# Performance work log

Hardware: AMD Instinct MI355X
Metric: run time of the kernel (lower is better)

Reference implementation:

```python
import jax, jax.numpy as jnp
import numpy as np


def setup_inputs() -> dict:
    key = jax.random.key(0)
    k1, k2 = jax.random.split(key)
    B, S, D = 8, 4096, 1024
    E, P = 8, 4
    x = jax.random.normal(k1, (B, S, D), dtype=jnp.float32)
    phi_kernel = jax.random.normal(k2, (D, E * P), dtype=jnp.float32) * (1.0 / np.sqrt(D))
    phi_bias = jnp.zeros((E * P,), dtype=jnp.float32)
    return {"x": x, "phi_kernel": phi_kernel, "phi_bias": phi_bias,
            "num_experts": E, "num_slots": P}


def reference(x, phi_kernel, phi_bias, num_experts, num_slots):
    B, S, D = x.shape
    E, P = num_experts, num_slots
    # phi logits: [B,S,E,P]
    phi_logits = (jnp.einsum('bsd,dk->bsk', x, phi_kernel) + phi_bias).reshape(B, S, E, P)
    # softmax over the sequence axis (each slot is a convex combo of tokens)
    phi_weights = jax.nn.softmax(phi_logits, axis=1)
    # soft slots: weighted sum over tokens -> [B,E,P,D] (fused, no [B,S,E,P,D] blowup)
    soft_slots = jnp.einsum('bsd,bsep->bepd', x, phi_weights)
    expert_inputs = soft_slots.reshape(B, E, P * D)
    expert_weights = jnp.full((B, S, E), 1.0 / E, dtype=x.dtype)
    expert_indices = jnp.broadcast_to(jnp.arange(E, dtype=jnp.int32)[None, None, :], (B, S, E))
    return (expert_weights, expert_indices, phi_weights, soft_slots, expert_inputs)
```

## Files before the change

kernel.cpp:

```cpp
#include <hip/hip_runtime.h>
#include <hip/hip_bf16.h>

#define B 8
#define S 4096
#define DD 1024
#define KK 32

template <int DSPLIT>
__global__ __launch_bounds__(256) void k1_logits(const float* __restrict__ x,
                                                 const float* __restrict__ phi,
                                                 float* __restrict__ lp) {
    constexpr int DCH = DD / DSPLIT;
    constexpr int NCH = DCH / 32;
    __shared__ float xt[128 * 36];

    const int bid = blockIdx.x;
    const int dq  = bid & (DSPLIT - 1);
    const int st  = (bid / DSPLIT) & 31;
    const int b   = bid / (DSPLIT * 32);
    const int s0  = st * 128;
    const int tid = threadIdx.x;
    const int kg  = __builtin_amdgcn_readfirstlane(tid >> 6);
    const int lane = tid & 63;

    float acc0[8], acc1[8];
#pragma unroll
    for (int j = 0; j < 8; ++j) { acc0[j] = 0.f; acc1[j] = 0.f; }

    const float* xb = x + ((size_t)(b * S + s0)) * DD + dq * DCH;

    for (int ch = 0; ch < NCH; ++ch) {
        __syncthreads();
#pragma unroll
        for (int i = 0; i < 4; ++i) {
            int f = tid + i * 256;
            int row = f >> 3;
            int c4 = f & 7;
            float4 v = *(const float4*)(xb + (size_t)row * DD + ch * 32 + c4 * 4);
            *(float4*)(xt + row * 36 + c4 * 4) = v;
        }
        __syncthreads();

        const float* pbase = phi + (size_t)(dq * DCH + ch * 32) * KK + kg * 8;
#pragma unroll
        for (int g = 0; g < 8; ++g) {
            float4 a0 = *(const float4*)(xt + lane * 36 + g * 4);
            float4 a1 = *(const float4*)(xt + (lane + 64) * 36 + g * 4);
            const float* a0p = &a0.x;
            const float* a1p = &a1.x;
#pragma unroll
            for (int dd = 0; dd < 4; ++dd) {
                const float* pr = pbase + (size_t)(g * 4 + dd) * KK;
                float4 pA = *(const float4*)(pr);
                float4 pB = *(const float4*)(pr + 4);
                float av0 = a0p[dd];
                float av1 = a1p[dd];
                acc0[0] += av0 * pA.x; acc0[1] += av0 * pA.y;
                acc0[2] += av0 * pA.z; acc0[3] += av0 * pA.w;
                acc0[4] += av0 * pB.x; acc0[5] += av0 * pB.y;
                acc0[6] += av0 * pB.z; acc0[7] += av0 * pB.w;
                acc1[0] += av1 * pA.x; acc1[1] += av1 * pA.y;
                acc1[2] += av1 * pA.z; acc1[3] += av1 * pA.w;
                acc1[4] += av1 * pB.x; acc1[5] += av1 * pB.y;
                acc1[6] += av1 * pB.z; acc1[7] += av1 * pB.w;
            }
        }
    }

    float* o = lp + (((size_t)dq * B + b) * KK + kg * 8) * S + s0;
#pragma unroll
    for (int j = 0; j < 8; ++j) {
        o[(size_t)j * S + lane]      = acc0[j];
        o[(size_t)j * S + 64 + lane] = acc1[j];
    }
}

template <int DSPLIT>
__global__ __launch_bounds__(256) void k2_softmax(const float* __restrict__ lp,
                                                  const float* __restrict__ bias,
                                                  float* __restrict__ pw) {
    const int b = blockIdx.x >> 5;
    const int k = blockIdx.x & 31;
    const int tid = threadIdx.x;
    const int wave = tid >> 6, lane = tid & 63;
    const size_t base = ((size_t)b * KK + k) * S;
    const float bk = bias[k];

    float v[16];
    float m = -1e30f;
#pragma unroll
    for (int i = 0; i < 16; ++i) {
        int s = tid + i * 256;
        float t = bk;
#pragma unroll
        for (int p = 0; p < DSPLIT; ++p) t += lp[(size_t)p * (B * KK * S) + base + s];
        v[i] = t;
        m = fmaxf(m, t);
    }
#pragma unroll
    for (int off = 32; off >= 1; off >>= 1) m = fmaxf(m, __shfl_xor(m, off, 64));

    __shared__ float redm[4];
    __shared__ float reds[4];
    if (lane == 0) redm[wave] = m;
    __syncthreads();
    m = fmaxf(fmaxf(redm[0], redm[1]), fmaxf(redm[2], redm[3]));

    float ssum = 0.f;
#pragma unroll
    for (int i = 0; i < 16; ++i) {
        v[i] = __expf(v[i] - m);
        ssum += v[i];
    }
#pragma unroll
    for (int off = 32; off >= 1; off >>= 1) ssum += __shfl_xor(ssum, off, 64);
    if (lane == 0) reds[wave] = ssum;
    __syncthreads();
    ssum = reds[0] + reds[1] + reds[2] + reds[3];

    float r = 1.0f / ssum;
#pragma unroll
    for (int i = 0; i < 16; ++i) {
        int s = tid + i * 256;
        pw[((size_t)b * S + s) * KK + k] = v[i] * r;
    }
}

template <int SSPLIT>
__global__ __launch_bounds__(256) void k3_partial(const float* __restrict__ x,
                                                  const float* __restrict__ pw,
                                                  float* __restrict__ part) {
    constexpr int SCH = S / SSPLIT;
    const int bid = blockIdx.x;
    const int sc = bid % SSPLIT;
    const int dt = (bid / SSPLIT) & 3;
    const int b  = bid / (SSPLIT * 4);
    const int tid = threadIdx.x;
    const int kg = __builtin_amdgcn_readfirstlane(tid >> 6);
    const int lane = tid & 63;

    float4 acc[8];
#pragma unroll
    for (int j = 0; j < 8; ++j) acc[j] = make_float4(0.f, 0.f, 0.f, 0.f);

    const float* xb = x + ((size_t)(b * S + sc * SCH)) * DD + dt * 256 + lane * 4;
    const float* wb = pw + ((size_t)(b * S + sc * SCH)) * KK + kg * 8;

#pragma unroll 4
    for (int s = 0; s < SCH; ++s) {
        float4 xv = *(const float4*)(xb + (size_t)s * DD);
        const float* wr = wb + (size_t)s * KK;
        float4 wA = *(const float4*)(wr);
        float4 wB = *(const float4*)(wr + 4);
        acc[0].x += wA.x * xv.x; acc[0].y += wA.x * xv.y; acc[0].z += wA.x * xv.z; acc[0].w += wA.x * xv.w;
        acc[1].x += wA.y * xv.x; acc[1].y += wA.y * xv.y; acc[1].z += wA.y * xv.z; acc[1].w += wA.y * xv.w;
        acc[2].x += wA.z * xv.x; acc[2].y += wA.z * xv.y; acc[2].z += wA.z * xv.z; acc[2].w += wA.z * xv.w;
        acc[3].x += wA.w * xv.x; acc[3].y += wA.w * xv.y; acc[3].z += wA.w * xv.z; acc[3].w += wA.w * xv.w;
        acc[4].x += wB.x * xv.x; acc[4].y += wB.x * xv.y; acc[4].z += wB.x * xv.z; acc[4].w += wB.x * xv.w;
        acc[5].x += wB.y * xv.x; acc[5].y += wB.y * xv.y; acc[5].z += wB.y * xv.z; acc[5].w += wB.y * xv.w;
        acc[6].x += wB.z * xv.x; acc[6].y += wB.z * xv.y; acc[6].z += wB.z * xv.z; acc[6].w += wB.z * xv.w;
        acc[7].x += wB.w * xv.x; acc[7].y += wB.w * xv.y; acc[7].z += wB.w * xv.z; acc[7].w += wB.w * xv.w;
    }

    float* pp = part + (((size_t)sc * B + b) * KK + kg * 8) * DD + dt * 256 + lane * 4;
#pragma unroll
    for (int j = 0; j < 8; ++j) *(float4*)(pp + (size_t)j * DD) = acc[j];
}

template <int SSPLIT>
__global__ __launch_bounds__(256) void k4_finalize(const float* __restrict__ part,
                                                   float* __restrict__ out) {
    const int idx = blockIdx.x * 256 + threadIdx.x;
    const float4* p4 = (const float4*)part;

    float4 sv = p4[idx];
#pragma unroll
    for (int c = 1; c < SSPLIT; ++c) {
        float4 t = p4[(size_t)c * 65536 + idx];
        sv.x += t.x; sv.y += t.y; sv.z += t.z; sv.w += t.w;
    }

    ((float4*)(out + 1572864))[idx] = sv;
    ((float4*)(out + 1835008))[idx] = sv;

    ((float4*)out)[idx] = make_float4(0.125f, 0.125f, 0.125f, 0.125f);
    float base = (float)((idx * 4) & 7);
    ((float4*)(out + 262144))[idx] = make_float4(base, base + 1.f, base + 2.f, base + 3.f);
}

extern "C" void kernel_launch(void* const* d_in, const int* in_sizes, int n_in,
                              void* d_out, int out_size, void* d_ws, size_t ws_size,
                              hipStream_t stream) {
    const float* x    = (const float*)d_in[0];
    const float* phi  = (const float*)d_in[1];
    const float* bias = (const float*)d_in[2];
    float* out = (float*)d_out;

    float* lp   = (float*)d_ws;
    float* part = (float*)d_ws;
    float* pw   = out + 524288;

    if (ws_size >= (size_t)17 * 1024 * 1024) {
        k1_logits<4><<<dim3(B * 32 * 4), dim3(256), 0, stream>>>(x, phi, lp);
        k2_softmax<4><<<dim3(B * KK), dim3(256), 0, stream>>>(lp, bias, pw);
        k3_partial<16><<<dim3(B * 4 * 16), dim3(256), 0, stream>>>(x, pw, part);
        k4_finalize<16><<<dim3(256), dim3(256), 0, stream>>>(part, out);
    } else {
        k1_logits<2><<<dim3(B * 32 * 2), dim3(256), 0, stream>>>(x, phi, lp);
        k2_softmax<2><<<dim3(B * KK), dim3(256), 0, stream>>>(lp, bias, pw);
        k3_partial<8><<<dim3(B * 4 * 8), dim3(256), 0, stream>>>(x, pw, part);
        k4_finalize<8><<<dim3(256), dim3(256), 0, stream>>>(part, out);
    }
}
```

Baseline: 269.4 us.

## Restructure pipeline: double-buffered logits, split softmax, transposed weights, wider S-split

The logits kernel now uses 64-row tiles with a fixed 2-way D split, double-buffered shared-memory staging with register prefetch, and bias folded into the accumulator init. The single-block-per-column softmax is replaced by a two-stage partial max/sum kernel plus a normalize kernel that writes both a transposed weight copy and the row-major output through a shared tile. The weighted-sum kernel reads the transposed weights with vector loads and splits S 32 ways when the workspace allows. The aim is more parallelism in the softmax and better-coalesced weight reads, at the cost of an extra launch, an extra weight buffer, and a larger workspace requirement.

```diff
diff --git a/kernel.cpp b/kernel.cpp
--- a/kernel.cpp
+++ b/kernel.cpp
@@ -6,129 +6,164 @@
 #define DD 1024
 #define KK 32
 
-template <int DSPLIT>
 __global__ __launch_bounds__(256) void k1_logits(const float* __restrict__ x,
                                                  const float* __restrict__ phi,
+                                                 const float* __restrict__ bias,
                                                  float* __restrict__ lp) {
-    constexpr int DCH = DD / DSPLIT;
-    constexpr int NCH = DCH / 32;
-    __shared__ float xt[128 * 36];
+    constexpr int DCH = 512, NCH = 16;
+    __shared__ float xt[2][64 * 36];
 
     const int bid = blockIdx.x;
-    const int dq  = bid & (DSPLIT - 1);
-    const int st  = (bid / DSPLIT) & 31;
-    const int b   = bid / (DSPLIT * 32);
-    const int s0  = st * 128;
+    const int dq  = bid & 1;
+    const int st  = (bid >> 1) & 63;
+    const int b   = bid >> 7;
+    const int s0  = st * 64;
     const int tid = threadIdx.x;
     const int kg  = __builtin_amdgcn_readfirstlane(tid >> 6);
     const int lane = tid & 63;
 
-    float acc0[8], acc1[8];
-#pragma unroll
-    for (int j = 0; j < 8; ++j) { acc0[j] = 0.f; acc1[j] = 0.f; }
+    float acc[8];
+#pragma unroll
+    for (int j = 0; j < 8; ++j) acc[j] = (dq == 0) ? bias[kg * 8 + j] : 0.f;
 
     const float* xb = x + ((size_t)(b * S + s0)) * DD + dq * DCH;
+    const int row = tid >> 3;
+    const int c4  = tid & 7;
+
+    {
+        float4 p0 = *(const float4*)(xb + (size_t)row * DD + c4 * 4);
+        float4 p1 = *(const float4*)(xb + (size_t)(row + 32) * DD + c4 * 4);
+        *(float4*)(&xt[0][row * 36 + c4 * 4]) = p0;
+        *(float4*)(&xt[0][(row + 32) * 36 + c4 * 4]) = p1;
+    }
+    __syncthreads();
 
     for (int ch = 0; ch < NCH; ++ch) {
-        __syncthreads();
-#pragma unroll
-        for (int i = 0; i < 4; ++i) {
-            int f = tid + i * 256;
-            int row = f >> 3;
-            int c4 = f & 7;
-            float4 v = *(const float4*)(xb + (size_t)row * DD + ch * 32 + c4 * 4);
-            *(float4*)(xt + row * 36 + c4 * 4) = v;
-        }
-        __syncthreads();
+        const int cur = ch & 1;
+        float4 q0, q1;
+        if (ch + 1 < NCH) {
+            q0 = *(const float4*)(xb + (size_t)row * DD + (ch + 1) * 32 + c4 * 4);
+            q1 = *(const float4*)(xb + (size_t)(row + 32) * DD + (ch + 1) * 32 + c4 * 4);
+        }
 
         const float* pbase = phi + (size_t)(dq * DCH + ch * 32) * KK + kg * 8;
+        const float* xrow  = &xt[cur][lane * 36];
 #pragma unroll
         for (int g = 0; g < 8; ++g) {
-            float4 a0 = *(const float4*)(xt + lane * 36 + g * 4);
-            float4 a1 = *(const float4*)(xt + (lane + 64) * 36 + g * 4);
-            const float* a0p = &a0.x;
-            const float* a1p = &a1.x;
+            float4 a = *(const float4*)(xrow + g * 4);
+            const float* ap = &a.x;
 #pragma unroll
             for (int dd = 0; dd < 4; ++dd) {
                 const float* pr = pbase + (size_t)(g * 4 + dd) * KK;
-                float4 pA = *(const float4*)(pr);
+                float4 pA = *(const float4*)pr;
                 float4 pB = *(const float4*)(pr + 4);
-                float av0 = a0p[dd];
-                float av1 = a1p[dd];
-                acc0[0] += av0 * pA.x; acc0[1] += av0 * pA.y;
-                acc0[2] += av0 * pA.z; acc0[3] += av0 * pA.w;
-                acc0[4] += av0 * pB.x; acc0[5] += av0 * pB.y;
-                acc0[6] += av0 * pB.z; acc0[7] += av0 * pB.w;
-                acc1[0] += av1 * pA.x; acc1[1] += av1 * pA.y;
-                acc1[2] += av1 * pA.z; acc1[3] += av1 * pA.w;
-                acc1[4] += av1 * pB.x; acc1[5] += av1 * pB.y;
-                acc1[6] += av1 * pB.z; acc1[7] += av1 * pB.w;
+                float av = ap[dd];
+                acc[0] += av * pA.x; acc[1] += av * pA.y;
+                acc[2] += av * pA.z; acc[3] += av * pA.w;
+                acc[4] += av * pB.x; acc[5] += av * pB.y;
+                acc[6] += av * pB.z; acc[7] += av * pB.w;
             }
         }
+        __syncthreads();
+        if (ch + 1 < NCH) {
+            *(float4*)(&xt[cur ^ 1][row * 36 + c4 * 4]) = q0;
+            *(float4*)(&xt[cur ^ 1][(row + 32) * 36 + c4 * 4]) = q1;
+        }
+        __syncthreads();
     }
 
     float* o = lp + (((size_t)dq * B + b) * KK + kg * 8) * S + s0;
 #pragma unroll
-    for (int j = 0; j < 8; ++j) {
-        o[(size_t)j * S + lane]      = acc0[j];
-        o[(size_t)j * S + 64 + lane] = acc1[j];
-    }
-}
-
-template <int DSPLIT>
-__global__ __launch_bounds__(256) void k2_softmax(const float* __restrict__ lp,
-                                                  const float* __restrict__ bias,
-                                                  float* __restrict__ pw) {
-    const int b = blockIdx.x >> 5;
-    const int k = blockIdx.x & 31;
+    for (int j = 0; j < 8; ++j) o[(size_t)j * S + lane] = acc[j];
+}
+
+__global__ __launch_bounds__(256) void k2a_partial(const float* __restrict__ lp,
+                                                   float* __restrict__ pmax,
+                                                   float* __restrict__ psum) {
+    const int bid = blockIdx.x;
+    const int c  = bid & 7;
+    const int bk = bid >> 3;
     const int tid = threadIdx.x;
     const int wave = tid >> 6, lane = tid & 63;
-    const size_t base = ((size_t)b * KK + k) * S;
-    const float bk = bias[k];
-
-    float v[16];
-    float m = -1e30f;
-#pragma unroll
-    for (int i = 0; i < 16; ++i) {
-        int s = tid + i * 256;
-        float t = bk;
-#pragma unroll
-        for (int p = 0; p < DSPLIT; ++p) t += lp[(size_t)p * (B * KK * S) + base + s];
-        v[i] = t;
-        m = fmaxf(m, t);
-    }
+    const size_t base = (size_t)bk * S + c * 512;
+
+    float v0 = lp[base + tid]       + lp[1048576 + base + tid];
+    float v1 = lp[base + tid + 256] + lp[1048576 + base + tid + 256];
+
+    float m = fmaxf(v0, v1);
 #pragma unroll
     for (int off = 32; off >= 1; off >>= 1) m = fmaxf(m, __shfl_xor(m, off, 64));
-
-    __shared__ float redm[4];
-    __shared__ float reds[4];
-    if (lane == 0) redm[wave] = m;
-    __syncthreads();
-    m = fmaxf(fmaxf(redm[0], redm[1]), fmaxf(redm[2], redm[3]));
-
-    float ssum = 0.f;
-#pragma unroll
-    for (int i = 0; i < 16; ++i) {
-        v[i] = __expf(v[i] - m);
-        ssum += v[i];
-    }
-#pragma unroll
-    for (int off = 32; off >= 1; off >>= 1) ssum += __shfl_xor(ssum, off, 64);
-    if (lane == 0) reds[wave] = ssum;
-    __syncthreads();
-    ssum = reds[0] + reds[1] + reds[2] + reds[3];
-
-    float r = 1.0f / ssum;
-#pragma unroll
-    for (int i = 0; i < 16; ++i) {
-        int s = tid + i * 256;
-        pw[((size_t)b * S + s) * KK + k] = v[i] * r;
+    __shared__ float sm[4], sl[4];
+    if (lane == 0) sm[wave] = m;
+    __syncthreads();
+    const float M = fmaxf(fmaxf(sm[0], sm[1]), fmaxf(sm[2], sm[3]));
+
+    float l = __expf(v0 - M) + __expf(v1 - M);
+#pragma unroll
+    for (int off = 32; off >= 1; off >>= 1) l += __shfl_xor(l, off, 64);
+    if (lane == 0) sl[wave] = l;
+    __syncthreads();
+    if (tid == 0) {
+        pmax[bid] = M;
+        psum[bid] = sl[0] + sl[1] + sl[2] + sl[3];
+    }
+}
+
+__global__ __launch_bounds__(256) void k2c_norm(const float* __restrict__ lp,
+                                                const float* __restrict__ pmax,
+                                                const float* __restrict__ psum,
+                                                float* __restrict__ pwT,
+                                                float* __restrict__ pw_out) {
+    __shared__ float tile[128][33];
+    __shared__ float sM[32], sLinv[32];
+    const int b  = blockIdx.x >> 5;
+    const int sc = blockIdx.x & 31;
+    const int s0 = sc * 128;
+    const int tid = threadIdx.x;
+
+    if (tid < 32) {
+        const int k = tid;
+        float M = -1e30f, L = 0.f;
+#pragma unroll
+        for (int c = 0; c < 8; ++c) {
+            float mc = pmax[(b * KK + k) * 8 + c];
+            float lc = psum[(b * KK + k) * 8 + c];
+            float nM = fmaxf(M, mc);
+            L = L * __expf(M - nM) + lc * __expf(mc - nM);
+            M = nM;
+        }
+        sM[k] = M;
+        sLinv[k] = 1.0f / L;
+    }
+    __syncthreads();
+
+    const int sL = tid & 127;
+    const int kh = tid >> 7;
+#pragma unroll
+    for (int kk = 0; kk < 16; ++kk) {
+        const int k = kk * 2 + kh;
+        const size_t idx = ((size_t)b * KK + k) * S + s0 + sL;
+        float v = lp[idx] + lp[1048576 + idx];
+        float w = __expf(v - sM[k]) * sLinv[k];
+        pwT[idx] = w;
+        tile[sL][k] = w;
+    }
+    __syncthreads();
+
+    float* ob = pw_out + ((size_t)b * S + s0) * KK;
+#pragma unroll
+    for (int i = 0; i < 4; ++i) {
+        const int idx4 = tid + i * 256;
+        const int sl = idx4 >> 3, kq = idx4 & 7;
+        float4 v4 = make_float4(tile[sl][kq * 4 + 0], tile[sl][kq * 4 + 1],
+                                tile[sl][kq * 4 + 2], tile[sl][kq * 4 + 3]);
+        ((float4*)ob)[idx4] = v4;
     }
 }
 
 template <int SSPLIT>
 __global__ __launch_bounds__(256) void k3_partial(const float* __restrict__ x,
-                                                  const float* __restrict__ pw,
+                                                  const float* __restrict__ pwT,
                                                   float* __restrict__ part) {
     constexpr int SCH = S / SSPLIT;
     const int bid = blockIdx.x;
@@ -144,22 +179,22 @@
     for (int j = 0; j < 8; ++j) acc[j] = make_float4(0.f, 0.f, 0.f, 0.f);
 
     const float* xb = x + ((size_t)(b * S + sc * SCH)) * DD + dt * 256 + lane * 4;
-    const float* wb = pw + ((size_t)(b * S + sc * SCH)) * KK + kg * 8;
-
-#pragma unroll 4
-    for (int s = 0; s < SCH; ++s) {
-        float4 xv = *(const float4*)(xb + (size_t)s * DD);
-        const float* wr = wb + (size_t)s * KK;
-        float4 wA = *(const float4*)(wr);
-        float4 wB = *(const float4*)(wr + 4);
-        acc[0].x += wA.x * xv.x; acc[0].y += wA.x * xv.y; acc[0].z += wA.x * xv.z; acc[0].w += wA.x * xv.w;
-        acc[1].x += wA.y * xv.x; acc[1].y += wA.y * xv.y; acc[1].z += wA.y * xv.z; acc[1].w += wA.y * xv.w;
-        acc[2].x += wA.z * xv.x; acc[2].y += wA.z * xv.y; acc[2].z += wA.z * xv.z; acc[2].w += wA.z * xv.w;
-        acc[3].x += wA.w * xv.x; acc[3].y += wA.w * xv.y; acc[3].z += wA.w * xv.z; acc[3].w += wA.w * xv.w;
-        acc[4].x += wB.x * xv.x; acc[4].y += wB.x * xv.y; acc[4].z += wB.x * xv.z; acc[4].w += wB.x * xv.w;
-        acc[5].x += wB.y * xv.x; acc[5].y += wB.y * xv.y; acc[5].z += wB.y * xv.z; acc[5].w += wB.y * xv.w;
-        acc[6].x += wB.z * xv.x; acc[6].y += wB.z * xv.y; acc[6].z += wB.z * xv.z; acc[6].w += wB.z * xv.w;
-        acc[7].x += wB.w * xv.x; acc[7].y += wB.w * xv.y; acc[7].z += wB.w * xv.z; acc[7].w += wB.w * xv.w;
+    const float* wb = pwT + ((size_t)b * KK + kg * 8) * S + sc * SCH;
+
+    for (int ss = 0; ss < SCH / 4; ++ss) {
+        float4 wq[8];
+#pragma unroll
+        for (int j = 0; j < 8; ++j) wq[j] = *(const float4*)(wb + (size_t)j * S + ss * 4);
+#pragma unroll
+        for (int dd = 0; dd < 4; ++dd) {
+            float4 xv = *(const float4*)(xb + (size_t)(ss * 4 + dd) * DD);
+#pragma unroll
+            for (int j = 0; j < 8; ++j) {
+                float w = ((const float*)&wq[j])[dd];
+                acc[j].x += w * xv.x; acc[j].y += w * xv.y;
+                acc[j].z += w * xv.z; acc[j].w += w * xv.w;
+            }
+        }
     }
 
     float* pp = part + (((size_t)sc * B + b) * KK + kg * 8) * DD + dt * 256 + lane * 4;
@@ -182,7 +217,6 @@
 
     ((float4*)(out + 1572864))[idx] = sv;
     ((float4*)(out + 1835008))[idx] = sv;
-
     ((float4*)out)[idx] = make_float4(0.125f, 0.125f, 0.125f, 0.125f);
     float base = (float)((idx * 4) & 7);
     ((float4*)(out + 262144))[idx] = make_float4(base, base + 1.f, base + 2.f, base + 3.f);
@@ -197,18 +231,21 @@
     float* out = (float*)d_out;
 
     float* lp   = (float*)d_ws;
-    float* part = (float*)d_ws;
-    float* pw   = out + 524288;
-
-    if (ws_size >= (size_t)17 * 1024 * 1024) {
-        k1_logits<4><<<dim3(B * 32 * 4), dim3(256), 0, stream>>>(x, phi, lp);
-        k2_softmax<4><<<dim3(B * KK), dim3(256), 0, stream>>>(lp, bias, pw);
-        k3_partial<16><<<dim3(B * 4 * 16), dim3(256), 0, stream>>>(x, pw, part);
-        k4_finalize<16><<<dim3(256), dim3(256), 0, stream>>>(part, out);
+    float* pmax = lp + 2097152;
+    float* psum = lp + 2101248;
+    float* pwT  = lp + 2105344;
+    float* part = lp + 3153920;
+    float* pw_out = out + 524288;
+
+    k1_logits<<<dim3(1024), dim3(256), 0, stream>>>(x, phi, bias, lp);
+    k2a_partial<<<dim3(2048), dim3(256), 0, stream>>>(lp, pmax, psum);
+    k2c_norm<<<dim3(256), dim3(256), 0, stream>>>(lp, pmax, psum, pwT, pw_out);
+
+    if (ws_size >= (size_t)47 * 1024 * 1024) {
+        k3_partial<32><<<dim3(B * 4 * 32), dim3(256), 0, stream>>>(x, pwT, part);
+        k4_finalize<32><<<dim3(256), dim3(256), 0, stream>>>(part, out);
     } else {
-        k1_logits<2><<<dim3(B * 32 * 2), dim3(256), 0, stream>>>(x, phi, lp);
-        k2_softmax<2><<<dim3(B * KK), dim3(256), 0, stream>>>(lp, bias, pw);
-        k3_partial<8><<<dim3(B * 4 * 8), dim3(256), 0, stream>>>(x, pw, part);
+        k3_partial<8><<<dim3(B * 4 * 8), dim3(256), 0, stream>>>(x, pwT, part);
         k4_finalize<8><<<dim3(256), dim3(256), 0, stream>>>(part, out);
     }
 }
```

Measured after the change: 267.9 us. Within noise of the previous version (-0.6%).
